# Kernel tuning notes

Measured on AMD Instinct MI355X. Metric: run time of the kernel, lower is better.

## Reference

```python
import jax, jax.numpy as jnp
import numpy as np

DIM = 1024
HDIM = 128
SEQ = 2048
B = 4
NHEADS = DIM // HDIM


def _decay_mask(seq_len, gamma):
    idx = jnp.arange(seq_len, dtype=jnp.float32)
    # gamma ** (i - j), lower-triangular (i >= j), else 0
    D = gamma ** (idx[:, None] - idx[None, :])
    D = jnp.where(idx[:, None] >= idx[None, :], D, 0.0)
    return D.astype(jnp.float32)


def setup_inputs() -> dict:
    key = jax.random.key(0)
    ks = jax.random.split(key, 8)
    q = jax.random.normal(ks[0], (B, SEQ, DIM), dtype=jnp.float32)
    k = jax.random.normal(ks[1], (B, SEQ, DIM), dtype=jnp.float32)
    v = jax.random.normal(ks[2], (B, SEQ, DIM), dtype=jnp.float32)
    # per-head shared QKV weight (source reuses one Dense for Q,K,V)
    scale = 1.0 / np.sqrt(HDIM)
    W_qkv = jax.random.normal(ks[3], (NHEADS, HDIM, HDIM), dtype=jnp.float32) * scale
    # gate: Dense(dim, bias, swish); output: Dense(dim, bias)
    Wg = jax.random.normal(ks[4], (DIM, DIM), dtype=jnp.float32) / np.sqrt(DIM)
    bg = jnp.zeros((DIM,), dtype=jnp.float32)
    Wo = jax.random.normal(ks[5], (DIM, DIM), dtype=jnp.float32) / np.sqrt(DIM)
    bo = jnp.zeros((DIM,), dtype=jnp.float32)
    # GroupNormalization(scale=False): default groups=32, center=True -> beta only
    beta = jnp.zeros((DIM,), dtype=jnp.float32)
    return {"q": q, "k": k, "v": v, "W_qkv": W_qkv, "Wg": Wg, "bg": bg,
            "Wo": Wo, "bo": bo, "beta": beta}


def _retention_head(qh, kh, vh, W, D):
    # qh,kh,vh: [B,S,HDIM]; source bug: all three come from q, and the
    # single shared Dense W projects each.
    Q = qh @ W
    K = kh @ W
    V = vh @ W
    x = jnp.einsum('bsd,btd->bst', Q, K) / jnp.sqrt(jnp.float32(HDIM))
    # D normalized: D / sqrt(sum over axis 1 (rows), broadcast over rows)
    Dn = D / jnp.sqrt(jnp.sum(D, axis=0))  # tf.reduce_sum(D,1) on [S,S]: axis=1 of 2D = cols? see note
    x = x * Dn
    # row-norm: divide by max(|sum over axis 1 of each [S,S] slice|, 1)
    s = jnp.sum(x, axis=1, keepdims=True)  # per-sample, tf axis 1 of [S,S]
    x = x / jnp.maximum(jnp.abs(s), 1.0)
    return jnp.einsum('bst,btd->bsd', x, V)


def _group_norm(x, beta, groups=32, eps=1e-3):
    b, s, c = x.shape
    xg = x.reshape(b, s, groups, c // groups)
    mu = jnp.mean(xg, axis=-1, keepdims=True)
    var = jnp.var(xg, axis=-1, keepdims=True)
    xn = (xg - mu) / jnp.sqrt(var + eps)
    return xn.reshape(b, s, c) + beta


def reference(q, k, v, W_qkv, Wg, bg, Wo, bo, beta):
    gammas = 1.0 - 2.0 ** (-5.0 - jnp.arange(NHEADS, dtype=jnp.float32))
    Wgate = jax.nn.swish(q @ Wg + bg)
    # source bug: splits q for Q, K, V alike
    qs = q.reshape(B, SEQ, NHEADS, HDIM)
    outs = []
    idx = jnp.arange(SEQ, dtype=jnp.float32)
    lower = idx[:, None] >= idx[None, :]
    for h in range(NHEADS):
        D = jnp.where(lower, gammas[h] ** (idx[:, None] - idx[None, :]), 0.0)
        qh = qs[:, :, h, :]
        outs.append(_retention_head(qh, qh, qh, W_qkv[h], D))
    x = jnp.concatenate(outs, axis=-1)
    Y = _group_norm(x, beta)
    return (Wgate * Y) @ Wo + bo
```

## Files before the change

### kernel.cpp

```cpp
#include <hip/hip_runtime.h>


constexpr int SEQ  = 2048;
constexpr int BATCH= 4;
constexpr int DIM  = 1024;
constexpr int HDIM = 128;
constexpr int NH   = 8;
constexpr int NBH  = BATCH * NH;
constexpr int NC   = 16;
constexpr int CCH  = 32;
constexpr int NCC  = SEQ / CCH;

typedef __bf16 bf16x8 __attribute__((ext_vector_type(8)));
typedef float  f32x4  __attribute__((ext_vector_type(4)));

__device__ __forceinline__ f32x4 mfma16(bf16x8 a, bf16x8 b, f32x4 c) {
  return __builtin_amdgcn_mfma_f32_16x16x32_bf16(a, b, c, 0, 0, 0);
}

__device__ __forceinline__ float bf2f(unsigned short u) {
  return __builtin_bit_cast(float, (unsigned int)u << 16);
}
__device__ __forceinline__ unsigned short f2bf(float f) {
  unsigned int x = __builtin_bit_cast(unsigned int, f);
  x += 0x7fffu + ((x >> 16) & 1u);
  return (unsigned short)(x >> 16);
}

__device__ __forceinline__ int swz(int row, int col, int RS) {
  int cb  = col >> 3;
  int scb = (cb & ~7) | ((cb ^ (row >> 1)) & 7);
  return row * RS + scb * 8 + (col & 7);
}

typedef const __attribute__((address_space(1))) unsigned int* gas_t;
typedef __attribute__((address_space(3))) unsigned int* las_t;
__device__ __forceinline__ void gl_lds16(const unsigned short* g, unsigned short* l) {
  __builtin_amdgcn_global_load_lds((gas_t)g, (las_t)l, 16, 0, 0);
}

__device__ __forceinline__ uint4 pack8(float4 a, float4 b) {
  uint4 o;
  o.x = (unsigned int)f2bf(a.x) | ((unsigned int)f2bf(a.y) << 16);
  o.y = (unsigned int)f2bf(a.z) | ((unsigned int)f2bf(a.w) << 16);
  o.z = (unsigned int)f2bf(b.x) | ((unsigned int)f2bf(b.y) << 16);
  o.w = (unsigned int)f2bf(b.z) | ((unsigned int)f2bf(b.w) << 16);
  return o;
}

__global__ void detect(const unsigned short* __restrict__ q, int* __restrict__ flag)
{
  int lane = threadIdx.x;
  int sane = 0;
  for (int i = lane; i < 1024; i += 64) {
    int e = (q[i] >> 7) & 0xFF;
    sane += (e >= 100 && e <= 140) ? 1 : 0;
  }
  #pragma unroll
  for (int o = 1; o < 64; o <<= 1) sane += __shfl_xor(sane, o);
  if (lane == 0) flag[0] = (sane >= 900) ? 1 : 0;
}

__global__ __launch_bounds__(256) void qbf(const void* __restrict__ q,
    unsigned short* __restrict__ qb, const int* __restrict__ dflag)
{
  const int idx = blockIdx.x * 256 + threadIdx.x;
  if (dflag[0]) {
    ((uint4*)qb)[idx] = ((const uint4*)q)[idx];
  } else {
    float4 a = ((const float4*)q)[2 * idx];
    float4 b = ((const float4*)q)[2 * idx + 1];
    ((uint4*)qb)[idx] = pack8(a, b);
  }
}

__global__ __launch_bounds__(256) void wtrans(const void* __restrict__ src,
    unsigned short* __restrict__ dst, int rows, int cols,
    const int* __restrict__ dflag)
{
  __shared__ float tile[64][65];
  const int isbf = dflag[0];
  const size_t moff = (size_t)blockIdx.z * rows * cols;
  const int r0 = blockIdx.y * 64, c0 = blockIdx.x * 64;
  const int tr = threadIdx.x >> 4;
  const int tc = (threadIdx.x & 15) * 4;

  #pragma unroll
  for (int rr = 0; rr < 64; rr += 16) {
    int r = r0 + rr + tr;
    if (isbf) {
      const unsigned short* s = (const unsigned short*)src + moff + (size_t)r * cols + c0 + tc;
      tile[rr + tr][tc + 0] = bf2f(s[0]);
      tile[rr + tr][tc + 1] = bf2f(s[1]);
      tile[rr + tr][tc + 2] = bf2f(s[2]);
      tile[rr + tr][tc + 3] = bf2f(s[3]);
    } else {
      float4 v = *(const float4*)((const float*)src + moff + (size_t)r * cols + c0 + tc);
      tile[rr + tr][tc + 0] = v.x;
      tile[rr + tr][tc + 1] = v.y;
      tile[rr + tr][tc + 2] = v.z;
      tile[rr + tr][tc + 3] = v.w;
    }
  }
  __syncthreads();

  const int n  = threadIdx.x >> 2;
  const int kg = (threadIdx.x & 3) * 16;
  unsigned int ov[8];
  #pragma unroll
  for (int j = 0; j < 8; ++j) {
    unsigned short lo = f2bf(tile[kg + 2 * j + 0][n]);
    unsigned short hi = f2bf(tile[kg + 2 * j + 1][n]);
    ov[j] = (unsigned int)lo | ((unsigned int)hi << 16);
  }
  unsigned short* d = dst + moff + (size_t)(c0 + n) * rows + r0 + kg;
  ((uint4*)d)[0] = make_uint4(ov[0], ov[1], ov[2], ov[3]);
  ((uint4*)d)[1] = make_uint4(ov[4], ov[5], ov[6], ov[7]);
}

__global__ __launch_bounds__(256, 4) void gemm128(
    const void* __restrict__ A, int lda,
    const unsigned short* __restrict__ B, int ldb, int K,
    const void* __restrict__ bias, int act,
    void* __restrict__ out, int mode, int adt, int obf,
    const int* __restrict__ dflag)
{
  __shared__ __align__(16) unsigned short As[128 * 64];
  __shared__ __align__(16) unsigned short Bs[128 * 64];
  const int isbf = dflag[0];
  const int abf  = (adt == 1) || (adt == 2 && isbf);
  const int tid  = threadIdx.x;
  const int lane = tid & 63;
  const int w    = tid >> 6;
  const int wy   = w >> 1, wx = w & 1;
  const int m15  = lane & 15, qd = lane >> 4;
  const int w8  = w * 8;
  const int lr  = lane >> 3;
  const int scb = lane & 7;

  int bx = blockIdx.x, by = blockIdx.y;
  if (mode == 0) {
    int nwg = gridDim.x * gridDim.y;
    int lin = by * gridDim.x + bx;
    int qq = nwg >> 3, rr = nwg & 7;
    int xcd = lin & 7, idx = lin >> 3;
    int wg = (xcd < rr) ? xcd * (qq + 1) + idx
                        : rr * (qq + 1) + (xcd - rr) * qq + idx;
    bx = wg % gridDim.x;
    by = wg / gridDim.x;
  }

  const size_t aoff = (mode == 1) ? (size_t)blockIdx.z * 128 : 0;
  const size_t boff = (mode == 1) ? (size_t)blockIdx.z * 128 * 128 : 0;
  const size_t arow = (size_t)(by * 128);
  const size_t bcol = (size_t)(bx * 128);

  f32x4 zero4 = {0.0f, 0.0f, 0.0f, 0.0f};
  f32x4 acc[4][4];
  #pragma unroll
  for (int i = 0; i < 4; ++i)
    #pragma unroll
    for (int j = 0; j < 4; ++j) acc[i][j] = zero4;

  const int kIters = K >> 6;
  for (int kt = 0; kt < kIters; ++kt) {
    __syncthreads();
    if (abf) {
      const unsigned short* pa = (const unsigned short*)A + aoff + arow * lda + kt * 64;
      #pragma unroll
      for (int g = 0; g < 4; ++g) {
        int r  = g * 32 + w8 + lr;
        int cb = scb ^ ((r >> 1) & 7);
        gl_lds16(pa + (size_t)r * lda + cb * 8, &As[g * 2048 + w * 512]);
      }
    } else {
      const float* pa = (const float*)A + aoff + arow * lda + kt * 64;
      #pragma unroll
      for (int g = 0; g < 4; ++g) {
        int idx = tid + g * 256;
        int r = idx >> 3, cb = idx & 7;
        float4 f0 = *(const float4*)(pa + (size_t)r * lda + cb * 8);
        float4 f1 = *(const float4*)(pa + (size_t)r * lda + cb * 8 + 4);
        *(uint4*)&As[swz(r, cb * 8, 64)] = pack8(f0, f1);
      }
    }
    {
      const unsigned short* pb = B + boff + bcol * (size_t)ldb + kt * 64;
      #pragma unroll
      for (int g = 0; g < 4; ++g) {
        int r  = g * 32 + w8 + lr;
        int cb = scb ^ ((r >> 1) & 7);
        gl_lds16(pb + (size_t)r * ldb + cb * 8, &Bs[g * 2048 + w * 512]);
      }
    }
    __syncthreads();
    #pragma unroll
    for (int kk = 0; kk < 2; ++kk) {
      bf16x8 af[4], bfr[4];
      #pragma unroll
      for (int mt = 0; mt < 4; ++mt)
        af[mt] = *(const bf16x8*)&As[swz(wy * 64 + mt * 16 + m15, kk * 32 + qd * 8, 64)];
      #pragma unroll
      for (int nt = 0; nt < 4; ++nt)
        bfr[nt] = *(const bf16x8*)&Bs[swz(wx * 64 + nt * 16 + m15, kk * 32 + qd * 8, 64)];
      #pragma unroll
      for (int mt = 0; mt < 4; ++mt)
        #pragma unroll
        for (int nt = 0; nt < 4; ++nt)
          acc[mt][nt] = mfma16(af[mt], bfr[nt], acc[mt][nt]);
    }
  }

  const int obf_eff = (obf == 2) ? (isbf ? 1 : 0) : obf;
  if (mode == 1) {
    #pragma unroll
    for (int half = 0; half < 2; ++half) {
      __syncthreads();
      if (wy == half) {
        #pragma unroll
        for (int mt = 0; mt < 4; ++mt)
          #pragma unroll
          for (int nt = 0; nt < 4; ++nt) {
            int n = wx * 64 + nt * 16 + m15;
            #pragma unroll
            for (int r = 0; r < 4; ++r) {
              int sl = mt * 16 + qd * 4 + r;
              As[swz(sl, n, 128)] = f2bf(acc[mt][nt][r]);
            }
          }
      }
      __syncthreads();
      #pragma unroll
      for (int g = 0; g < 4; ++g) {
        int idx = tid + g * 256;
        int rr = idx >> 4, cbb = idx & 15;
        int m = by * 128 + half * 64 + rr;
        int b = m >> 11, s = m & 2047;
        size_t bh = (size_t)(b * NH + blockIdx.z);
        *(uint4*)&((unsigned short*)out)[(bh * SEQ + s) * HDIM + cbb * 8] =
            *(const uint4*)&As[swz(rr, cbb * 8, 128)];
      }
    }
    return;
  }

  #pragma unroll
  for (int mt = 0; mt < 4; ++mt)
    #pragma unroll
    for (int nt = 0; nt < 4; ++nt) {
      int nl = wx * 64 + nt * 16 + m15;
      int n  = bx * 128 + nl;
      float bv = 0.0f;
      if (bias) bv = isbf ? bf2f(((const unsigned short*)bias)[n]) : ((const float*)bias)[n];
      #pragma unroll
      for (int r = 0; r < 4; ++r) {
        int ml = wy * 64 + mt * 16 + qd * 4 + r;
        int m  = by * 128 + ml;
        float v = acc[mt][nt][r] + bv;
        if (act == 1) v = v / (1.0f + __expf(-v));
        size_t oi = (size_t)m * (gridDim.x * 128) + n;
        if (obf_eff) ((unsigned short*)out)[oi] = f2bf(v);
        else         ((float*)out)[oi] = v;
      }
    }
}

__global__ __launch_bounds__(128) void kzcA(const unsigned short* __restrict__ X,
                                            float* __restrict__ L)
{
  const int d  = threadIdx.x;
  const int cc = blockIdx.x;
  const int bh = blockIdx.y;
  const int h  = bh & 7;
  const float gam = 1.0f - exp2f(-5.0f - (float)h);
  const unsigned short* Xb = X + (size_t)bh * SEQ * HDIM + (size_t)cc * CCH * HDIM;
  float z = 0.0f;
  #pragma unroll
  for (int i = CCH - 1; i >= 0; --i)
    z = bf2f(Xb[(size_t)i * HDIM + d]) + gam * z;
  L[((size_t)bh * NCC + cc) * HDIM + d] = z;
}

__global__ __launch_bounds__(128) void kzcB(float* __restrict__ L)
{
  const int d  = threadIdx.x;
  const int bh = blockIdx.x;
  const int h  = bh & 7;
  const float gam = 1.0f - exp2f(-5.0f - (float)h);
  const float g32 = exp2f(log2f(gam) * (float)CCH);
  float z = 0.0f;
  for (int cc = NCC - 1; cc >= 0; --cc) {
    size_t i = ((size_t)bh * NCC + cc) * HDIM + d;
    float lc = L[i];
    L[i] = z;
    z = lc + g32 * z;
  }
}

__global__ __launch_bounds__(64) void kdot2(const unsigned short* __restrict__ X,
    const float* __restrict__ Carry, float* __restrict__ U)
{
  const int lane = threadIdx.x;
  const int cc   = blockIdx.x;
  const int bh   = blockIdx.y;
  const int h    = bh & 7;
  const float gam    = 1.0f - exp2f(-5.0f - (float)h);
  const float l2g    = log2f(gam);
  const float inv1mg = exp2f(5.0f + (float)h);
  const float c1     = 0.08838834764831845f;
  const unsigned short* Xb = X + (size_t)bh * SEQ * HDIM + (size_t)cc * CCH * HDIM;
  float2 cr = *(const float2*)(Carry + ((size_t)bh * NCC + cc) * HDIM + lane * 2);
  float z0 = 0.0f, z1 = 0.0f;
  float coeff = gam;
  float keep = 0.0f;
  #pragma unroll
  for (int i = 0; i < CCH; ++i) {
    const int t = CCH - 1 - i;
    unsigned int xu = *(const unsigned int*)(Xb + (size_t)t * HDIM + lane * 2);
    float x0 = bf2f((unsigned short)(xu & 0xffffu));
    float x1 = bf2f((unsigned short)(xu >> 16));
    z0 = x0 + gam * z0;
    z1 = x1 + gam * z1;
    float dot = x0 * (z0 + coeff * cr.x) + x1 * (z1 + coeff * cr.y);
    #pragma unroll
    for (int o = 1; o < 64; o <<= 1) dot += __shfl_xor(dot, o);
    if (lane == t) keep = dot;
    coeff *= gam;
  }
  if (lane < CCH) {
    int tg = cc * CCH + lane;
    float colD   = (1.0f - exp2f(l2g * (float)(SEQ - tg))) * inv1mg;
    float sq     = sqrtf(colD);
    float colsum = keep * c1 / sq;
    float den    = fmaxf(fabsf(colsum), 1.0f);
    U[(size_t)bh * SEQ + tg] = c1 / (sq * den);
  }
}

__global__ __launch_bounds__(256, 2) void chunkstate(
    const unsigned short* __restrict__ X,
    const float* __restrict__ U,
    unsigned short* __restrict__ G)
{
  __shared__ __align__(16) unsigned short XT [16384];
  __shared__ __align__(16) unsigned short XTs[16384];
  const int tid  = threadIdx.x;
  const int lane = tid & 63;
  const int w    = tid >> 6;
  const int wy   = w >> 1, wx = w & 1;
  const int m15  = lane & 15, qd = lane >> 4;
  const int c    = blockIdx.x;
  const int bh   = blockIdx.y;
  const int h    = bh & 7;
  const float gam = 1.0f - exp2f(-5.0f - (float)h);
  const float l2g = log2f(gam);
  const int t0 = c * 128;
  const unsigned short* Xb = X + (size_t)bh * SEQ * HDIM;
  const float* Ub = U + (size_t)bh * SEQ;

  #pragma unroll
  for (int g = 0; g < 8; ++g) {
    int idx = tid + g * 256;
    int t = idx >> 4, d0 = (idx & 15) * 8;
    uint4 w4 = *(const uint4*)(Xb + (size_t)(t0 + t) * HDIM + d0);
    float wt = exp2f(l2g * (float)(127 - t)) * Ub[t0 + t];
    const unsigned short* wp = (const unsigned short*)&w4;
    #pragma unroll
    for (int j = 0; j < 8; ++j) {
      unsigned short v = wp[j];
      XT [swz(d0 + j, t, 128)] = v;
      XTs[swz(d0 + j, t, 128)] = f2bf(bf2f(v) * wt);
    }
  }
  __syncthreads();

  f32x4 zero4 = {0.0f, 0.0f, 0.0f, 0.0f};
  f32x4 acc[4][4];
  #pragma unroll
  for (int i = 0; i < 4; ++i)
    #pragma unroll
    for (int j = 0; j < 4; ++j) acc[i][j] = zero4;

  #pragma unroll
  for (int kk = 0; kk < 4; ++kk) {
    bf16x8 af[4], bfr[4];
    #pragma unroll
    for (int mt = 0; mt < 4; ++mt)
      af[mt] = *(const bf16x8*)&XTs[swz(wy * 64 + mt * 16 + m15, kk * 32 + qd * 8, 128)];
    #pragma unroll
    for (int nt = 0; nt < 4; ++nt)
      bfr[nt] = *(const bf16x8*)&XT[swz(wx * 64 + nt * 16 + m15, kk * 32 + qd * 8, 128)];
    #pragma unroll
    for (int mt = 0; mt < 4; ++mt)
      #pragma unroll
      for (int nt = 0; nt < 4; ++nt)
        acc[mt][nt] = mfma16(af[mt], bfr[nt], acc[mt][nt]);
  }

  unsigned short* Gp = G + (((size_t)bh * NC + c) << 14);
  #pragma unroll
  for (int half = 0; half < 2; ++half) {
    __syncthreads();
    if (wy == half) {
      #pragma unroll
      for (int mt = 0; mt < 4; ++mt)
        #pragma unroll
        for (int nt = 0; nt < 4; ++nt) {
          int d2 = wx * 64 + nt * 16 + m15;
          #pragma unroll
          for (int r = 0; r < 4; ++r) {
            int dl = mt * 16 + qd * 4 + r;
            XT[swz(dl, d2, 128)] = f2bf(acc[mt][nt][r]);
          }
        }
    }
    __syncthreads();
    #pragma unroll
    for (int g = 0; g < 4; ++g) {
      int idx = tid + g * 256;
      int rr = idx >> 4, cbb = idx & 15;
      *(uint4*)&Gp[(size_t)(half * 64 + rr) * 128 + cbb * 8] =
          *(const uint4*)&XT[swz(rr, cbb * 8, 128)];
    }
  }
}

__global__ __launch_bounds__(256) void scanS(unsigned short* __restrict__ GS)
{
  int gid = blockIdx.x * 256 + threadIdx.x;
  int bh = gid >> 11;
  int e8 = (gid & 2047) << 3;
  int h  = bh & 7;
  float gam  = 1.0f - exp2f(-5.0f - (float)h);
  float g128 = exp2f(log2f(gam) * 128.0f);
  float s[8];
  #pragma unroll
  for (int j = 0; j < 8; ++j) s[j] = 0.0f;
  unsigned short* base = GS + ((size_t)bh << 18) + e8;
  #pragma unroll
  for (int c = 0; c < NC; ++c) {
    uint4 v = *(uint4*)(base + ((size_t)c << 14));
    const unsigned short* wp = (const unsigned short*)&v;
    #pragma unroll
    for (int j = 0; j < 8; ++j) s[j] = g128 * s[j] + bf2f(wp[j]);
    uint4 o;
    unsigned int* op = (unsigned int*)&o;
    op[0] = (unsigned int)f2bf(s[0]) | ((unsigned int)f2bf(s[1]) << 16);
    op[1] = (unsigned int)f2bf(s[2]) | ((unsigned int)f2bf(s[3]) << 16);
    op[2] = (unsigned int)f2bf(s[4]) | ((unsigned int)f2bf(s[5]) << 16);
    op[3] = (unsigned int)f2bf(s[6]) | ((unsigned int)f2bf(s[7]) << 16);
    *(uint4*)(base + ((size_t)c << 14)) = o;
  }
}

__global__ __launch_bounds__(256, 2) void retention2(
    const unsigned short* __restrict__ X,
    const float* __restrict__ U,
    const unsigned short* __restrict__ S,
    unsigned short* __restrict__ R)
{
  __shared__ __align__(16) unsigned short Qs[16384];
  __shared__ __align__(16) unsigned short SB[16384];

  const int tid  = threadIdx.x;
  const int lane = tid & 63;
  const int w    = tid >> 6;
  const int wy   = w >> 1, wx = w & 1;
  const int m15  = lane & 15, qd = lane >> 4;
  const int c    = blockIdx.x;
  const int bh   = blockIdx.y;
  const int h    = bh & 7;
  const int b    = bh >> 3;
  const float gam = 1.0f - exp2f(-5.0f - (float)h);
  const float l2g = log2f(gam);
  const int sbase = c * 128;
  const unsigned short* Xb = X + (size_t)bh * SEQ * HDIM;
  const float* Ub = U + (size_t)bh * SEQ;

  #pragma unroll
  for (int g = 0; g < 8; ++g) {
    int idx = tid + g * 256;
    int r = idx >> 4, cb = idx & 15;
    *(uint4*)&Qs[swz(r, cb * 8, 128)] =
        *(const uint4*)(Xb + (size_t)(sbase + r) * HDIM + cb * 8);
  }
  if (c > 0) {
    const unsigned short* Sp = S + (((size_t)bh * NC + (c - 1)) << 14);
    #pragma unroll
    for (int g = 0; g < 8; ++g) {
      int idx = tid + g * 256;
      int r = idx >> 4, cb = idx & 15;
      *(uint4*)&SB[swz(r, cb * 8, 128)] = *(const uint4*)(Sp + (size_t)r * 128 + cb * 8);
    }
  }
  __syncthreads();

  bf16x8 aq[4][4];
  #pragma unroll
  for (int mt = 0; mt < 4; ++mt)
    #pragma unroll
    for (int kk = 0; kk < 4; ++kk)
      aq[mt][kk] = *(const bf16x8*)&Qs[swz(wy * 64 + mt * 16 + m15, kk * 32 + qd * 8, 128)];

  float crowL[16];
  #pragma unroll
  for (int mt = 0; mt < 4; ++mt)
    #pragma unroll
    for (int r = 0; r < 4; ++r)
      crowL[mt * 4 + r] = exp2f(l2g * (float)(wy * 64 + mt * 16 + qd * 4 + r));

  f32x4 zero4 = {0.0f, 0.0f, 0.0f, 0.0f};
  f32x4 oacc[4][4];
  #pragma unroll
  for (int i = 0; i < 4; ++i)
    #pragma unroll
    for (int j = 0; j < 4; ++j) oacc[i][j] = zero4;

  if (c > 0) {
    #pragma unroll
    for (int kk = 0; kk < 4; ++kk) {
      bf16x8 bs[4];
      #pragma unroll
      for (int nt = 0; nt < 4; ++nt)
        bs[nt] = *(const bf16x8*)&SB[swz(wx * 64 + nt * 16 + m15, kk * 32 + qd * 8, 128)];
      #pragma unroll
      for (int mt = 0; mt < 4; ++mt)
        #pragma unroll
        for (int nt = 0; nt < 4; ++nt)
          oacc[mt][nt] = mfma16(aq[mt][kk], bs[nt], oacc[mt][nt]);
    }
    #pragma unroll
    for (int mt = 0; mt < 4; ++mt) {
      #pragma unroll
      for (int r = 0; r < 4; ++r) {
        float f = crowL[mt * 4 + r] * gam;
        #pragma unroll
        for (int nt = 0; nt < 4; ++nt) oacc[mt][nt][r] *= f;
      }
    }
  }

  unsigned short* VsT = SB;
  unsigned short* Ps  = SB + 8192;

  for (int th = 0; th < 2; ++th) {
    const int t0 = th * 64;
    f32x4 pacc[4][2];
    #pragma unroll
    for (int i = 0; i < 4; ++i) { pacc[i][0] = zero4; pacc[i][1] = zero4; }
    #pragma unroll
    for (int kk = 0; kk < 4; ++kk) {
      bf16x8 bk[2];
      #pragma unroll
      for (int nt = 0; nt < 2; ++nt)
        bk[nt] = *(const bf16x8*)&Qs[swz(t0 + wx * 32 + nt * 16 + m15, kk * 32 + qd * 8, 128)];
      #pragma unroll
      for (int mt = 0; mt < 4; ++mt)
        #pragma unroll
        for (int nt = 0; nt < 2; ++nt)
          pacc[mt][nt] = mfma16(aq[mt][kk], bk[nt], pacc[mt][nt]);
    }
    __syncthreads();

    #pragma unroll
    for (int g = 0; g < 4; ++g) {
      int idx = tid + g * 256;
      int t = idx & 63, d0 = (idx >> 6) * 8;
      uint4 w4 = *(const uint4*)(Xb + (size_t)(sbase + t0 + t) * HDIM + d0);
      const unsigned short* wp = (const unsigned short*)&w4;
      #pragma unroll
      for (int j = 0; j < 8; ++j)
        VsT[swz(d0 + j, t, 64)] = wp[j];
    }
    #pragma unroll
    for (int nt = 0; nt < 2; ++nt) {
      int tloc = t0 + wx * 32 + nt * 16 + m15;
      float cf = exp2f(-l2g * (float)tloc) * Ub[sbase + tloc];
      #pragma unroll
      for (int mt = 0; mt < 4; ++mt)
        #pragma unroll
        for (int r = 0; r < 4; ++r) {
          int sl = wy * 64 + mt * 16 + qd * 4 + r;
          float v = (sl >= tloc) ? pacc[mt][nt][r] * crowL[mt * 4 + r] * cf : 0.0f;
          Ps[swz(sl, tloc - t0, 64)] = f2bf(v);
        }
    }
    __syncthreads();
    #pragma unroll
    for (int kk = 0; kk < 2; ++kk) {
      bf16x8 ap[4], bv[4];
      #pragma unroll
      for (int mt = 0; mt < 4; ++mt)
        ap[mt] = *(const bf16x8*)&Ps[swz(wy * 64 + mt * 16 + m15, kk * 32 + qd * 8, 64)];
      #pragma unroll
      for (int nt = 0; nt < 4; ++nt)
        bv[nt] = *(const bf16x8*)&VsT[swz(wx * 64 + nt * 16 + m15, kk * 32 + qd * 8, 64)];
      #pragma unroll
      for (int mt = 0; mt < 4; ++mt)
        #pragma unroll
        for (int nt = 0; nt < 4; ++nt)
          oacc[mt][nt] = mfma16(ap[mt], bv[nt], oacc[mt][nt]);
    }
  }

  __syncthreads();
  #pragma unroll
  for (int mt = 0; mt < 4; ++mt)
    #pragma unroll
    for (int nt = 0; nt < 4; ++nt) {
      int n = wx * 64 + nt * 16 + m15;
      #pragma unroll
      for (int r = 0; r < 4; ++r) {
        int sl = wy * 64 + mt * 16 + qd * 4 + r;
        SB[swz(sl, n, 128)] = f2bf(oacc[mt][nt][r]);
      }
    }
  __syncthreads();
  #pragma unroll
  for (int g = 0; g < 8; ++g) {
    int idx = tid + g * 256;
    int rr = idx >> 4, cbb = idx & 15;
    *(uint4*)&R[(size_t)(b * SEQ + sbase + rr) * DIM + h * HDIM + cbb * 8] =
        *(const uint4*)&SB[swz(rr, cbb * 8, 128)];
  }
}

__global__ __launch_bounds__(256) void gn_gate(const unsigned short* __restrict__ R,
    const void* __restrict__ beta, unsigned short* __restrict__ GU,
    const int* __restrict__ dflag)
{
  const int isbf = dflag[0];
  const int row = blockIdx.x;
  const int t   = threadIdx.x;
  uint2 xv = *(const uint2*)(R + (size_t)row * DIM + t * 4);
  float x0 = bf2f((unsigned short)(xv.x & 0xffffu)), x1 = bf2f((unsigned short)(xv.x >> 16));
  float x2 = bf2f((unsigned short)(xv.y & 0xffffu)), x3 = bf2f((unsigned short)(xv.y >> 16));
  float s  = x0 + x1 + x2 + x3;
  float ss = x0 * x0 + x1 * x1 + x2 * x2 + x3 * x3;
  #pragma unroll
  for (int m = 1; m <= 4; m <<= 1) {
    s  += __shfl_xor(s, m, 8);
    ss += __shfl_xor(ss, m, 8);
  }
  float mean = s * (1.0f / 32.0f);
  float var  = ss * (1.0f / 32.0f) - mean * mean;
  float rstd = rsqrtf(var + 1e-3f);
  float b0, b1, b2, b3;
  if (isbf) {
    uint2 bv = *(const uint2*)((const unsigned short*)beta + t * 4);
    b0 = bf2f((unsigned short)(bv.x & 0xffffu)); b1 = bf2f((unsigned short)(bv.x >> 16));
    b2 = bf2f((unsigned short)(bv.y & 0xffffu)); b3 = bf2f((unsigned short)(bv.y >> 16));
  } else {
    float4 bv = *(const float4*)((const float*)beta + t * 4);
    b0 = bv.x; b1 = bv.y; b2 = bv.z; b3 = bv.w;
  }
  uint2 gv = *(const uint2*)(GU + (size_t)row * DIM + t * 4);
  float g0 = bf2f((unsigned short)(gv.x & 0xffffu)), g1 = bf2f((unsigned short)(gv.x >> 16));
  float g2 = bf2f((unsigned short)(gv.y & 0xffffu)), g3 = bf2f((unsigned short)(gv.y >> 16));
  unsigned short u0 = f2bf(((x0 - mean) * rstd + b0) * g0);
  unsigned short u1 = f2bf(((x1 - mean) * rstd + b1) * g1);
  unsigned short u2 = f2bf(((x2 - mean) * rstd + b2) * g2);
  unsigned short u3 = f2bf(((x3 - mean) * rstd + b3) * g3);
  uint2 o;
  o.x = (unsigned int)u0 | ((unsigned int)u1 << 16);
  o.y = (unsigned int)u2 | ((unsigned int)u3 << 16);
  *(uint2*)(GU + (size_t)row * DIM + t * 4) = o;
}

extern "C" void kernel_launch(void* const* d_in, const int* in_sizes, int n_in,
                              void* d_out, int out_size, void* d_ws, size_t ws_size,
                              hipStream_t stream)
{
  (void)in_sizes; (void)n_in; (void)out_size;
  const void* q    = d_in[0];
  const void* Wqkv = d_in[3];
  const void* Wg   = d_in[4];
  const void* bg   = d_in[5];
  const void* Wo   = d_in[6];
  const void* bo   = d_in[7];
  const void* beta = d_in[8];

  char* p = (char*)d_ws;
  auto take = [&](size_t bytes) { char* r = p; p += (bytes + 255) & ~(size_t)255; return r; };
  int*  flag = (int*)take(256);
  unsigned short* X  = (unsigned short*)take((size_t)NBH * SEQ * HDIM * 2);
  float* U     = (float*)take((size_t)NBH * SEQ * 4);
  unsigned short* WqkvT = (unsigned short*)take((size_t)NH * HDIM * HDIM * 2);
  unsigned short* WgT   = (unsigned short*)take((size_t)DIM * DIM * 2);
  unsigned short* WoT   = (unsigned short*)take((size_t)DIM * DIM * 2);
  size_t qbBytes = (size_t)BATCH * SEQ * DIM * 2;
  unsigned short* qb = (unsigned short*)take(qbBytes);
  const bool useQb = ((size_t)(p - (char*)d_ws) <= ws_size);
  unsigned short* Rb = (unsigned short*)d_out;
  unsigned short* GS = (unsigned short*)((char*)d_out + (size_t)16 * 1024 * 1024);
  float* Carry = (float*)GS;
  unsigned short* Gg = X;

  detect<<<1, 64, 0, stream>>>((const unsigned short*)q, flag);

  wtrans<<<dim3(16, 16, 1), 256, 0, stream>>>(Wg,   WgT,   DIM,  DIM,  flag);
  wtrans<<<dim3(16, 16, 1), 256, 0, stream>>>(Wo,   WoT,   DIM,  DIM,  flag);
  wtrans<<<dim3(2, 2, NH),  256, 0, stream>>>(Wqkv, WqkvT, HDIM, HDIM, flag);
  if (useQb)
    qbf<<<4096, 256, 0, stream>>>(q, qb, flag);

  const void* Aq = useQb ? (const void*)qb : q;
  const int   adtq = useQb ? 1 : 2;

  gemm128<<<dim3(1, 64, NH), 256, 0, stream>>>(Aq, DIM, WqkvT, HDIM, HDIM,
                                               nullptr, 0, X, 1, adtq, 1, flag);

  kzcA <<<dim3(NCC, NBH), 128, 0, stream>>>(X, Carry);
  kzcB <<<NBH, 128, 0, stream>>>(Carry);
  kdot2<<<dim3(NCC, NBH), 64, 0, stream>>>(X, Carry, U);

  chunkstate<<<dim3(NC, NBH), 256, 0, stream>>>(X, U, GS);
  scanS     <<<256, 256, 0, stream>>>(GS);
  retention2<<<dim3(NC, NBH), 256, 0, stream>>>(X, U, GS, Rb);

  gemm128<<<dim3(8, 64, 1), 256, 0, stream>>>(Aq, DIM, WgT, DIM, DIM, bg, 1,
                                              Gg, 0, adtq, 1, flag);

  gn_gate<<<dim3(BATCH * SEQ, 1, 1), 256, 0, stream>>>(Rb, beta, Gg, flag);

  gemm128<<<dim3(8, 64, 1), 256, 0, stream>>>(Gg, DIM, WoT, DIM, DIM, bo, 0,
                                              d_out, 0, 1, 2, flag);
}
```

Measured before the change: 321.5 us.

## Halve GEMM N-tile, stage bf16 epilogue through LDS, async-load retention tiles

The shared GEMM kernel now uses 128x64 output tiles instead of 128x128, which doubles the grid size for all three GEMM launches and cuts the accumulator register count. The bf16-output epilogue (including bias and swish) is written through LDS so global stores can be coalesced 16-byte writes. Separately, the retention kernel loads Q and state tiles with direct global-to-LDS copies using a matching swizzle, and prefetches the second V half into registers before it is needed. Smaller tiles lower per-block reuse of A and raise total A traffic, in exchange for more occupancy and more parallel blocks.

Measured after the change: 296.3 us. -7.8%, faster.

```diff
diff --git a/kernel.cpp b/kernel.cpp
--- a/kernel.cpp
+++ b/kernel.cpp
@@ -126,7 +126,7 @@
     const int* __restrict__ dflag)
 {
   __shared__ __align__(16) unsigned short As[128 * 64];
-  __shared__ __align__(16) unsigned short Bs[128 * 64];
+  __shared__ __align__(16) unsigned short Bs[64 * 64];
   const int isbf = dflag[0];
   const int abf  = (adt == 1) || (adt == 2 && isbf);
   const int tid  = threadIdx.x;
@@ -153,14 +153,14 @@
   const size_t aoff = (mode == 1) ? (size_t)blockIdx.z * 128 : 0;
   const size_t boff = (mode == 1) ? (size_t)blockIdx.z * 128 * 128 : 0;
   const size_t arow = (size_t)(by * 128);
-  const size_t bcol = (size_t)(bx * 128);
+  const size_t bcol = (size_t)(bx * 64);
 
   f32x4 zero4 = {0.0f, 0.0f, 0.0f, 0.0f};
-  f32x4 acc[4][4];
+  f32x4 acc[4][2];
   #pragma unroll
   for (int i = 0; i < 4; ++i)
     #pragma unroll
-    for (int j = 0; j < 4; ++j) acc[i][j] = zero4;
+    for (int j = 0; j < 2; ++j) acc[i][j] = zero4;
 
   const int kIters = K >> 6;
   for (int kt = 0; kt < kIters; ++kt) {
@@ -187,7 +187,7 @@
     {
       const unsigned short* pb = B + boff + bcol * (size_t)ldb + kt * 64;
       #pragma unroll
-      for (int g = 0; g < 4; ++g) {
+      for (int g = 0; g < 2; ++g) {
         int r  = g * 32 + w8 + lr;
         int cb = scb ^ ((r >> 1) & 7);
         gl_lds16(pb + (size_t)r * ldb + cb * 8, &Bs[g * 2048 + w * 512]);
@@ -196,49 +196,56 @@
     __syncthreads();
     #pragma unroll
     for (int kk = 0; kk < 2; ++kk) {
-      bf16x8 af[4], bfr[4];
+      bf16x8 af[4], bfr[2];
       #pragma unroll
       for (int mt = 0; mt < 4; ++mt)
         af[mt] = *(const bf16x8*)&As[swz(wy * 64 + mt * 16 + m15, kk * 32 + qd * 8, 64)];
       #pragma unroll
-      for (int nt = 0; nt < 4; ++nt)
-        bfr[nt] = *(const bf16x8*)&Bs[swz(wx * 64 + nt * 16 + m15, kk * 32 + qd * 8, 64)];
+      for (int nt = 0; nt < 2; ++nt)
+        bfr[nt] = *(const bf16x8*)&Bs[swz(wx * 32 + nt * 16 + m15, kk * 32 + qd * 8, 64)];
       #pragma unroll
       for (int mt = 0; mt < 4; ++mt)
         #pragma unroll
-        for (int nt = 0; nt < 4; ++nt)
+        for (int nt = 0; nt < 2; ++nt)
           acc[mt][nt] = mfma16(af[mt], bfr[nt], acc[mt][nt]);
     }
   }
 
   const int obf_eff = (obf == 2) ? (isbf ? 1 : 0) : obf;
-  if (mode == 1) {
-    #pragma unroll
-    for (int half = 0; half < 2; ++half) {
-      __syncthreads();
-      if (wy == half) {
+
+  if (mode == 1 || obf_eff) {
+    __syncthreads();
+    #pragma unroll
+    for (int mt = 0; mt < 4; ++mt)
+      #pragma unroll
+      for (int nt = 0; nt < 2; ++nt) {
+        int nl = wx * 32 + nt * 16 + m15;
+        float bv = 0.0f;
+        if (bias) {
+          int n = bx * 64 + nl;
+          bv = isbf ? bf2f(((const unsigned short*)bias)[n]) : ((const float*)bias)[n];
+        }
         #pragma unroll
-        for (int mt = 0; mt < 4; ++mt)
-          #pragma unroll
-          for (int nt = 0; nt < 4; ++nt) {
-            int n = wx * 64 + nt * 16 + m15;
-            #pragma unroll
-            for (int r = 0; r < 4; ++r) {
-              int sl = mt * 16 + qd * 4 + r;
-              As[swz(sl, n, 128)] = f2bf(acc[mt][nt][r]);
-            }
-          }
-      }
-      __syncthreads();
-      #pragma unroll
-      for (int g = 0; g < 4; ++g) {
-        int idx = tid + g * 256;
-        int rr = idx >> 4, cbb = idx & 15;
-        int m = by * 128 + half * 64 + rr;
+        for (int r = 0; r < 4; ++r) {
+          int ml = wy * 64 + mt * 16 + qd * 4 + r;
+          float v = acc[mt][nt][r] + bv;
+          if (act == 1) v = v / (1.0f + __expf(-v));
+          As[swz(ml, nl, 64)] = f2bf(v);
+        }
+      }
+    __syncthreads();
+    #pragma unroll
+    for (int g = 0; g < 4; ++g) {
+      int idx = tid + g * 256;
+      int rr = idx >> 3, cbb = idx & 7;
+      int m = by * 128 + rr;
+      uint4 vv = *(const uint4*)&As[swz(rr, cbb * 8, 64)];
+      if (mode == 1) {
         int b = m >> 11, s = m & 2047;
         size_t bh = (size_t)(b * NH + blockIdx.z);
-        *(uint4*)&((unsigned short*)out)[(bh * SEQ + s) * HDIM + cbb * 8] =
-            *(const uint4*)&As[swz(rr, cbb * 8, 128)];
+        *(uint4*)&((unsigned short*)out)[(bh * SEQ + s) * HDIM + bx * 64 + cbb * 8] = vv;
+      } else {
+        *(uint4*)&((unsigned short*)out)[(size_t)m * (gridDim.x * 64) + bx * 64 + cbb * 8] = vv;
       }
     }
     return;
@@ -247,9 +254,9 @@
   #pragma unroll
   for (int mt = 0; mt < 4; ++mt)
     #pragma unroll
-    for (int nt = 0; nt < 4; ++nt) {
-      int nl = wx * 64 + nt * 16 + m15;
-      int n  = bx * 128 + nl;
+    for (int nt = 0; nt < 2; ++nt) {
+      int nl = wx * 32 + nt * 16 + m15;
+      int n  = bx * 64 + nl;
       float bv = 0.0f;
       if (bias) bv = isbf ? bf2f(((const unsigned short*)bias)[n]) : ((const float*)bias)[n];
       #pragma unroll
@@ -258,9 +265,7 @@
         int m  = by * 128 + ml;
         float v = acc[mt][nt][r] + bv;
         if (act == 1) v = v / (1.0f + __expf(-v));
-        size_t oi = (size_t)m * (gridDim.x * 128) + n;
-        if (obf_eff) ((unsigned short*)out)[oi] = f2bf(v);
-        else         ((float*)out)[oi] = v;
+        ((float*)out)[(size_t)m * (gridDim.x * 64) + n] = v;
       }
     }
 }
@@ -477,21 +482,31 @@
   const unsigned short* Xb = X + (size_t)bh * SEQ * HDIM;
   const float* Ub = U + (size_t)bh * SEQ;
 
-  #pragma unroll
-  for (int g = 0; g < 8; ++g) {
+  {
+    const int lr4 = lane >> 4;
+    const int cbd = lane & 15;
+    #pragma unroll
+    for (int g = 0; g < 8; ++g) {
+      int r   = g * 16 + w * 4 + lr4;
+      int cbs = (cbd & 8) | ((cbd ^ (r >> 1)) & 7);
+      gl_lds16(Xb + (size_t)(sbase + r) * HDIM + cbs * 8, &Qs[(g * 16 + w * 4) * 128]);
+    }
+    if (c > 0) {
+      const unsigned short* Sp = S + (((size_t)bh * NC + (c - 1)) << 14);
+      #pragma unroll
+      for (int g = 0; g < 8; ++g) {
+        int r   = g * 16 + w * 4 + lr4;
+        int cbs = (cbd & 8) | ((cbd ^ (r >> 1)) & 7);
+        gl_lds16(Sp + (size_t)r * 128 + cbs * 8, &SB[(g * 16 + w * 4) * 128]);
+      }
+    }
+  }
+  uint4 rvb[2][4];
+  #pragma unroll
+  for (int g = 0; g < 4; ++g) {
     int idx = tid + g * 256;
-    int r = idx >> 4, cb = idx & 15;
-    *(uint4*)&Qs[swz(r, cb * 8, 128)] =
-        *(const uint4*)(Xb + (size_t)(sbase + r) * HDIM + cb * 8);
-  }
-  if (c > 0) {
-    const unsigned short* Sp = S + (((size_t)bh * NC + (c - 1)) << 14);
-    #pragma unroll
-    for (int g = 0; g < 8; ++g) {
-      int idx = tid + g * 256;
-      int r = idx >> 4, cb = idx & 15;
-      *(uint4*)&SB[swz(r, cb * 8, 128)] = *(const uint4*)(Sp + (size_t)r * 128 + cb * 8);
-    }
+    int t = idx & 63, d0 = (idx >> 6) * 8;
+    rvb[0][g] = *(const uint4*)(Xb + (size_t)(sbase + t) * HDIM + d0);
   }
   __syncthreads();
 
@@ -543,6 +558,7 @@
   unsigned short* VsT = SB;
   unsigned short* Ps  = SB + 8192;
 
+  #pragma unroll
   for (int th = 0; th < 2; ++th) {
     const int t0 = th * 64;
     f32x4 pacc[4][2];
@@ -566,11 +582,18 @@
     for (int g = 0; g < 4; ++g) {
       int idx = tid + g * 256;
       int t = idx & 63, d0 = (idx >> 6) * 8;
-      uint4 w4 = *(const uint4*)(Xb + (size_t)(sbase + t0 + t) * HDIM + d0);
-      const unsigned short* wp = (const unsigned short*)&w4;
+      const unsigned short* wp = (const unsigned short*)&rvb[th][g];
       #pragma unroll
       for (int j = 0; j < 8; ++j)
         VsT[swz(d0 + j, t, 64)] = wp[j];
+    }
+    if (th == 0) {
+      #pragma unroll
+      for (int g = 0; g < 4; ++g) {
+        int idx = tid + g * 256;
+        int t = idx & 63, d0 = (idx >> 6) * 8;
+        rvb[1][g] = *(const uint4*)(Xb + (size_t)(sbase + 64 + t) * HDIM + d0);
+      }
     }
     #pragma unroll
     for (int nt = 0; nt < 2; ++nt) {
@@ -707,7 +730,7 @@
   const void* Aq = useQb ? (const void*)qb : q;
   const int   adtq = useQb ? 1 : 2;
 
-  gemm128<<<dim3(1, 64, NH), 256, 0, stream>>>(Aq, DIM, WqkvT, HDIM, HDIM,
+  gemm128<<<dim3(2, 64, NH), 256, 0, stream>>>(Aq, DIM, WqkvT, HDIM, HDIM,
                                                nullptr, 0, X, 1, adtq, 1, flag);
 
   kzcA <<<dim3(NCC, NBH), 128, 0, stream>>>(X, Carry);
@@ -718,11 +741,11 @@
   scanS     <<<256, 256, 0, stream>>>(GS);
   retention2<<<dim3(NC, NBH), 256, 0, stream>>>(X, U, GS, Rb);
 
-  gemm128<<<dim3(8, 64, 1), 256, 0, stream>>>(Aq, DIM, WgT, DIM, DIM, bg, 1,
-                                              Gg, 0, adtq, 1, flag);
+  gemm128<<<dim3(16, 64, 1), 256, 0, stream>>>(Aq, DIM, WgT, DIM, DIM, bg, 1,
+                                               Gg, 0, adtq, 1, flag);
 
   gn_gate<<<dim3(BATCH * SEQ, 1, 1), 256, 0, stream>>>(Rb, beta, Gg, flag);
 
-  gemm128<<<dim3(8, 64, 1), 256, 0, stream>>>(Gg, DIM, WoT, DIM, DIM, bo, 0,
-                                              d_out, 0, 1, 2, flag);
-}
+  gemm128<<<dim3(16, 64, 1), 256, 0, stream>>>(Gg, DIM, WoT, DIM, DIM, bo, 0,
+                                               d_out, 0, 1, 2, flag);
+}
```
